# Kernel tuning notes

Measured on AMD Instinct MI355X. Metric: run time of the kernel, lower is better.

Reference implementation:

```python
import jax, jax.numpy as jnp
import numpy as np

KS = 3          # deformable kernel size
N = KS * KS     # 9 sampling points
PAD = 1         # zero padding before sampling


def setup_inputs() -> dict:
    key = jax.random.key(0)
    k = jax.random.split(key, 4)
    b, c, h, w = 8, 64, 128, 128
    x = jax.random.normal(k[0], (b, c, h, w), jnp.float32)
    # offset-prediction conv: Conv2d(c, 2*N, 3, padding=1, stride=1) with bias
    w_off = jax.random.normal(k[1], (2 * N, c, 3, 3), jnp.float32) * 0.01
    b_off = jax.random.normal(k[2], (2 * N,), jnp.float32) * 0.01
    # main conv: Conv2d(c, c, 3, stride=3, bias=None) applied to rearranged samples
    w_conv = jax.random.normal(k[3], (c, c, KS, KS), jnp.float32) * (1.0 / np.sqrt(c * N))
    return {"x": x, "w_off": w_off, "b_off": b_off, "w_conv": w_conv}


def _deform_conv2d(x, w_off, b_off, w_conv):
    b, c, h, w = x.shape
    # 1) predict offsets: (b, 2N, h, w)
    offset = jax.lax.conv_general_dilated(
        x, w_off, (1, 1), ((PAD, PAD), (PAD, PAD)),
        dimension_numbers=("NCHW", "OIHW", "NCHW"))
    offset = offset + b_off[None, :, None, None]
    offset = offset.transpose(0, 2, 3, 1)  # (b, h, w, 2N), first N = rows, last N = cols

    # 2) sampling positions p = p_0 + p_n + offset (in zero-padded coords)
    dx, dy = jnp.meshgrid(
        jnp.arange(-(KS - 1) // 2, (KS - 1) // 2 + 1),
        jnp.arange(-(KS - 1) // 2, (KS - 1) // 2 + 1), indexing="ij")
    pn_x = dx.reshape(-1).astype(x.dtype)  # (N,)
    pn_y = dy.reshape(-1).astype(x.dtype)
    r0 = jnp.arange(1, h + 1, dtype=x.dtype)  # p_0 starts at 1 (padding shift)
    c0 = jnp.arange(1, w + 1, dtype=x.dtype)
    p_x = offset[..., :N] + pn_x + r0[None, :, None, None]   # (b,h,w,N)
    p_y = offset[..., N:] + pn_y + c0[None, None, :, None]

    xp = jnp.pad(x, ((0, 0), (0, 0), (PAD, PAD), (PAD, PAD)))
    Hp, Wp = h + 2 * PAD, w + 2 * PAD

    fx = jnp.floor(p_x)
    fy = jnp.floor(p_y)
    q_lt_x = jnp.clip(fx, 0, Hp - 1).astype(jnp.int32)
    q_lt_y = jnp.clip(fy, 0, Wp - 1).astype(jnp.int32)
    q_rb_x = jnp.clip(fx + 1, 0, Hp - 1).astype(jnp.int32)
    q_rb_y = jnp.clip(fy + 1, 0, Wp - 1).astype(jnp.int32)
    p_x = jnp.clip(p_x, 0, Hp - 1)
    p_y = jnp.clip(p_y, 0, Wp - 1)

    # bilinear weights (b,h,w,N); q values are non-differentiable (int)
    g_lt = (1 + (q_lt_x - p_x)) * (1 + (q_lt_y - p_y))
    g_rb = (1 - (q_rb_x - p_x)) * (1 - (q_rb_y - p_y))
    g_lb = (1 + (q_lt_x - p_x)) * (1 - (q_rb_y - p_y))
    g_rt = (1 - (q_rb_x - p_x)) * (1 + (q_lt_y - p_y))

    xp_flat = xp.reshape(b, c, Hp * Wp)

    def gather(qx, qy):
        idx = (qx * Wp + qy).reshape(b, 1, h * w * N)
        out = jnp.take_along_axis(
            xp_flat, jnp.broadcast_to(idx, (b, c, h * w * N)), axis=2)
        return out.reshape(b, c, h, w, N)

    x_off = (g_lt[:, None] * gather(q_lt_x, q_lt_y)
             + g_rb[:, None] * gather(q_rb_x, q_rb_y)
             + g_lb[:, None] * gather(q_lt_x, q_rb_y)
             + g_rt[:, None] * gather(q_rb_x, q_lt_y))  # (b,c,h,w,N)

    # 3) final KSxKS conv with stride KS over the rearranged samples is exactly
    #    a contraction over the N sampling points (sample n = kernel tap (i,j), n=i*KS+j)
    out = jnp.einsum("bchwn,ocn->bohw", x_off, w_conv.reshape(c, c, N))
    return out


def reference(x, w_off, b_off, w_conv):
    return _deform_conv2d(x, w_off, b_off, w_conv) + x
```

## Files before the change

### kernel.cpp

```cpp
#include <hip/hip_runtime.h>


typedef _Float16 h2    __attribute__((ext_vector_type(2)));
typedef _Float16 f16x8 __attribute__((ext_vector_type(8)));
typedef float    f32x4 __attribute__((ext_vector_type(4)));

#define MFMAH(a, b, c) __builtin_amdgcn_mfma_f32_16x16x32_f16(a, b, c, 0, 0, 0)

__device__ __forceinline__ unsigned short f2h(float f) {
    return __builtin_bit_cast(unsigned short, (_Float16)f);
}
__device__ __forceinline__ float h2f_bits(unsigned u) {
    return (float)__builtin_bit_cast(_Float16, (unsigned short)(u & 0xffffu));
}
__device__ __forceinline__ unsigned dup16(float g) {
    _Float16 t = (_Float16)g;
    h2 r = {t, t};
    return __builtin_bit_cast(unsigned, r);
}

__device__ __forceinline__ void blend8(const uint4* clo, const uint4* chi, uint4 gq,
                                       f16x8& bfr0, f16x8& bfr1) {
    h2 g0 = __builtin_bit_cast(h2, gq.x), g1 = __builtin_bit_cast(h2, gq.y);
    h2 g2 = __builtin_bit_cast(h2, gq.z), g3 = __builtin_bit_cast(h2, gq.w);
    const unsigned* c0 = (const unsigned*)&clo[0];
    const unsigned* c1 = (const unsigned*)&clo[1];
    const unsigned* c2 = (const unsigned*)&clo[2];
    const unsigned* c3 = (const unsigned*)&clo[3];
    const unsigned* e0 = (const unsigned*)&chi[0];
    const unsigned* e1 = (const unsigned*)&chi[1];
    const unsigned* e2 = (const unsigned*)&chi[2];
    const unsigned* e3 = (const unsigned*)&chi[3];
    unsigned owl[4], owh[4];
#pragma unroll
    for (int d = 0; d < 4; ++d) {
        h2 sl = __builtin_bit_cast(h2, c0[d]) * g0;
        sl = __builtin_elementwise_fma(__builtin_bit_cast(h2, c1[d]), g1, sl);
        sl = __builtin_elementwise_fma(__builtin_bit_cast(h2, c2[d]), g2, sl);
        sl = __builtin_elementwise_fma(__builtin_bit_cast(h2, c3[d]), g3, sl);
        owl[d] = __builtin_bit_cast(unsigned, sl);
        h2 sh = __builtin_bit_cast(h2, e0[d]) * g0;
        sh = __builtin_elementwise_fma(__builtin_bit_cast(h2, e1[d]), g1, sh);
        sh = __builtin_elementwise_fma(__builtin_bit_cast(h2, e2[d]), g2, sh);
        sh = __builtin_elementwise_fma(__builtin_bit_cast(h2, e3[d]), g3, sh);
        owh[d] = __builtin_bit_cast(unsigned, sh);
    }
    bfr0 = __builtin_bit_cast(f16x8, *(const uint4*)owl);
    bfr1 = __builtin_bit_cast(f16x8, *(const uint4*)owh);
}

__global__ __launch_bounds__(256) void k_prep_xt(const float* __restrict__ x,
                                                 unsigned short* __restrict__ xt) {
    __shared__ float xs[64][129];
    const int bh = blockIdx.x;
    const int h = bh & 127, b = bh >> 7;
    const float* xr = x + ((size_t)b * 64 * 128 + h) * 128;
    for (int idx = threadIdx.x; idx < 8192; idx += 256) {
        int c = idx >> 7, w = idx & 127;
        xs[c][w] = xr[(size_t)c * 16384 + w];
    }
    __syncthreads();
    unsigned short* xto = xt + ((size_t)bh << 13);
    for (int j = threadIdx.x; j < 1024; j += 256) {
        int w = j >> 3, c0 = (j & 7) << 3;
        unsigned short tmp[8];
#pragma unroll
        for (int e = 0; e < 8; ++e) tmp[e] = f2h(xs[c0 + e][w]);
        *(uint4*)(xto + w * 64 + c0) = *(const uint4*)tmp;
    }
}

__global__ void k_prep_w(const float* __restrict__ w_conv, const float* __restrict__ w_off,
                         unsigned short* __restrict__ w_m2, unsigned short* __restrict__ woff2) {
    int t = blockIdx.x * 256 + threadIdx.x;
    if (t < 36864) {
        int r = t & 511;
        int fid = t >> 9;
        int l15 = r >> 5, q4 = (r >> 3) & 3, e = t & 7;
        int chunk = fid & 1, of = (fid >> 1) & 3, n = fid >> 3;
        int o = of * 16 + l15, c = chunk * 32 + q4 * 8 + e;
        w_m2[t] = f2h(w_conv[(o * 64 + c) * 9 + n]);
    }
    int t2 = t - 36864;
    if (t2 >= 0 && t2 < 18432) {
        int r = t2 & 511;
        int fid = t2 >> 9;
        int l15 = r >> 5, q4 = (r >> 3) & 3, e = t2 & 7;
        int kc = fid & 1, half = (fid >> 1) & 1, rj = fid >> 2;
        int k = half * 16 + l15, c = kc * 32 + q4 * 8 + e;
        woff2[t2] = (k < 18) ? f2h(w_off[(k * 64 + c) * 9 + rj]) : (unsigned short)0;
    }
}

__global__ __launch_bounds__(256, 2) void k_fused(
    const float* __restrict__ x, const unsigned short* __restrict__ xt,
    const unsigned short* __restrict__ w_m2, const unsigned short* __restrict__ woff2,
    const float* __restrict__ b_off, float* __restrict__ out) {

    __shared__ __align__(16) unsigned char raw[6 * 70 * 128];
    __shared__ __align__(16) _Float16 offv[64 * 24];
    __shared__ int sfb;

    const int wk = ((blockIdx.x & 7) << 8) + (blockIdx.x >> 3);
    const int b = wk >> 8, h = (wk >> 1) & 127, wt = (wk & 1) << 6;

    const int tid  = threadIdx.x;
    const int lane = tid & 63, wid = tid >> 6;
    const int l15  = lane & 15, q4 = lane >> 4;
    const int lofs = ((l15 << 2) + q4) << 3;
    const int px   = wid * 16 + l15;

    const unsigned short* xtb = xt + ((size_t)b << 20);
    const _Float16* wmh  = (const _Float16*)w_m2;
    const _Float16* wofh = (const _Float16*)woff2;

    if (tid == 0) sfb = 0;

    for (int idx = tid; idx < 3360; idx += 256) {
        int rec = idx >> 3, cc = idx & 7;
        int rl = rec / 70, col = rec - rl * 70;
        int xr = h - 2 + rl, xc = wt - 3 + col;
        uint4 v = make_uint4(0, 0, 0, 0);
        if (xr >= 0 && xr < 128 && xc >= 0 && xc < 128)
            v = *(const uint4*)(xtb + ((((size_t)xr << 7) + xc) << 6) + (cc << 3));
        *(uint4*)(raw + (rec << 7) + ((cc ^ (col & 7)) << 4)) = v;
    }
    __syncthreads();

    {
        f32x4 o0a = {0,0,0,0}, o0b = {0,0,0,0}, o1a = {0,0,0,0}, o1b = {0,0,0,0};
        f16x8 bfgA, af0A, af1A, bfgB, af0B, af1B;

#define ALOAD(s, S)                                                                      \
        {                                                                                \
            constexpr int rj = (s) >> 1, kc = (s) & 1;                                   \
            const int colw = px + (rj % 3) + 2;                                          \
            const int recb = ((rj / 3) + 1) * 70 + colw;                                 \
            bfg##S = *(const f16x8*)(raw + (recb << 7) + ((((kc << 2) + q4) ^ (colw & 7)) << 4)); \
            af0##S = *(const f16x8*)(wofh + ((((rj * 2 + 0) << 1) + kc) << 9) + lofs);   \
            af1##S = *(const f16x8*)(wofh + ((((rj * 2 + 1) << 1) + kc) << 9) + lofs);   \
        }
#define AEXEC(S, P)                                                                      \
        {                                                                                \
            o0##P = MFMAH(af0##S, bfg##S, o0##P);                                        \
            o1##P = MFMAH(af1##S, bfg##S, o1##P);                                        \
        }
        ALOAD(0, A)
        ALOAD(1, B)  AEXEC(A, a)
        ALOAD(2, A)  AEXEC(B, b)
        ALOAD(3, B)  AEXEC(A, a)
        ALOAD(4, A)  AEXEC(B, b)
        ALOAD(5, B)  AEXEC(A, a)
        ALOAD(6, A)  AEXEC(B, b)
        ALOAD(7, B)  AEXEC(A, a)
        ALOAD(8, A)  AEXEC(B, b)
        ALOAD(9, B)  AEXEC(A, a)
        ALOAD(10, A) AEXEC(B, b)
        ALOAD(11, B) AEXEC(A, a)
        ALOAD(12, A) AEXEC(B, b)
        ALOAD(13, B) AEXEC(A, a)
        ALOAD(14, A) AEXEC(B, b)
        ALOAD(15, B) AEXEC(A, a)
        ALOAD(16, A) AEXEC(B, b)
        ALOAD(17, B) AEXEC(A, a)
                     AEXEC(B, b)
#undef ALOAD
#undef AEXEC
        f32x4 o0, o1;
#pragma unroll
        for (int rg = 0; rg < 4; ++rg) { o0[rg] = o0a[rg] + o0b[rg]; o1[rg] = o1a[rg] + o1b[rg]; }
        float4 bo = *(const float4*)(b_off + (q4 << 2));
        float2 bo2 = *(const float2*)(b_off + 16);
        const float bov[4] = {bo.x, bo.y, bo.z, bo.w};
#pragma unroll
        for (int rg = 0; rg < 4; ++rg) {
            int o = (q4 << 2) + rg;
            offv[px * 24 + o] = (_Float16)(o0[rg] + bov[rg]);
            if (q4 == 0 && rg < 2) offv[px * 24 + 16 + rg] = (_Float16)(o1[rg] + (rg ? bo2.y : bo2.x));
        }
    }
    __syncthreads();

    for (int idx = tid; idx < 576; idx += 256) {
        const int n = idx >> 6, p = idx & 63;
        const int g = n / 3, dj = n % 3;
        float ox = (float)offv[p * 24 + n], oy = (float)offv[p * 24 + 9 + n];
        float pxf = (float)(h + g) + ox, pyf = (float)(wt + p + dj) + oy;
        float fx = floorf(pxf), fy = floorf(pyf);
        int wr0 = (int)fminf(fmaxf(fx, 0.f), 129.f) + 1 - h;
        int wr1 = (int)fminf(fmaxf(fx + 1.f, 0.f), 129.f) + 1 - h;
        int c0 = (int)fminf(fmaxf(fy, 0.f), 129.f) - wt + 2;
        int c1 = (int)fminf(fmaxf(fy + 1.f, 0.f), 129.f) - wt + 2;
        bool oow = ((unsigned)wr0 > 5u) | ((unsigned)wr1 > 5u) |
                   ((unsigned)c0 > 69u) | ((unsigned)c1 > 69u);
        if (oow) sfb = 1;
    }
    __syncthreads();
    const bool slow = (sfb != 0);

    const size_t obase = ((size_t)b * 64 * 128 + h) * 128 + wt + px;
    float xres[4][4];
#pragma unroll
    for (int of = 0; of < 4; ++of)
#pragma unroll
        for (int rg = 0; rg < 4; ++rg)
            xres[of][rg] = x[obase + (size_t)((of << 4) + (q4 << 2) + rg) * 16384];

    f32x4 acc[4];
#pragma unroll
    for (int of = 0; of < 4; ++of) acc[of] = (f32x4){0.f, 0.f, 0.f, 0.f};

    if (!slow) {
        const unsigned* op = (const unsigned*)(offv + px * 24);
        uint4 oA = *(const uint4*)op;
        uint4 oB = *(const uint4*)(op + 4);
        unsigned oC = op[8];
        const unsigned owr[9] = {oA.x, oA.y, oA.z, oA.w, oB.x, oB.y, oB.z, oB.w, oC};
#define OXQ(n) h2f_bits(owr[(n) >> 1] >> (((n) & 1) << 4))
#define OYQ(n) h2f_bits(owr[(9 + (n)) >> 1] >> (((9 + (n)) & 1) << 4))

        uint4 cloA[4], chiA[4], cloB[4], chiB[4];
        uint4 gqA, gqB;
        f16x8 waA[8], waB[8];

#define TAPLOAD(n, S)                                                                    \
        {                                                                                \
            constexpr int g = (n) / 3, dj = (n) % 3;                                     \
            float ox = OXQ(n), oy = OYQ(n);                                              \
            float pxf = (float)(h + g) + ox, pyf = (float)(wt + px + dj) + oy;           \
            float fx = floorf(pxf), fy = floorf(pyf);                                    \
            float qx0f = fminf(fmaxf(fx, 0.f), 129.f);                                   \
            float qx1f = fminf(fmaxf(fx + 1.f, 0.f), 129.f);                             \
            float qy0f = fminf(fmaxf(fy, 0.f), 129.f);                                   \
            float qy1f = fminf(fmaxf(fy + 1.f, 0.f), 129.f);                             \
            float pxc = fminf(fmaxf(pxf, 0.f), 129.f);                                   \
            float pyc = fminf(fmaxf(pyf, 0.f), 129.f);                                   \
            float ax0 = 1.f + (qx0f - pxc), ax1 = 1.f - (qx1f - pxc);                    \
            float ay0 = 1.f + (qy0f - pyc), ay1 = 1.f - (qy1f - pyc);                    \
            int r0 = ((int)qx0f + 1 - h) * 70, r1 = ((int)qx1f + 1 - h) * 70;            \
            int c0 = (int)qy0f - wt + 2, c1 = (int)qy1f - wt + 2;                        \
            int blt = (r0 + c0) << 7, brb = (r1 + c1) << 7;                              \
            int blb = (r0 + c1) << 7, brt = (r1 + c0) << 7;                              \
            int z0 = ((q4 ^ c0) & 7) << 4, z1 = ((q4 ^ c1) & 7) << 4;                    \
            clo##S[0] = *(const uint4*)(raw + blt + z0);                                 \
            chi##S[0] = *(const uint4*)(raw + blt + (z0 ^ 64));                          \
            clo##S[1] = *(const uint4*)(raw + brb + z1);                                 \
            chi##S[1] = *(const uint4*)(raw + brb + (z1 ^ 64));                          \
            clo##S[2] = *(const uint4*)(raw + blb + z1);                                 \
            chi##S[2] = *(const uint4*)(raw + blb + (z1 ^ 64));                          \
            chi##S[3] = *(const uint4*)(raw + brt + (z0 ^ 64));                          \
            clo##S[3] = *(const uint4*)(raw + brt + z0);                                 \
            gq##S = make_uint4(dup16(ax0 * ay0), dup16(ax1 * ay1),                       \
                               dup16(ax0 * ay1), dup16(ax1 * ay0));                      \
            const _Float16* wn = wmh + ((n) << 12);                                      \
            _Pragma("unroll")                                                            \
            for (int of = 0; of < 4; ++of) {                                             \
                wa##S[2 * of]     = *(const f16x8*)(wn + (((of << 1) + 0) << 9) + lofs); \
                wa##S[2 * of + 1] = *(const f16x8*)(wn + (((of << 1) + 1) << 9) + lofs); \
            }                                                                            \
        }

#define TAPEXEC(S)                                                                       \
        {                                                                                \
            f16x8 bfr0, bfr1;                                                            \
            blend8(clo##S, chi##S, gq##S, bfr0, bfr1);                                   \
            _Pragma("unroll")                                                            \
            for (int of = 0; of < 4; ++of) {                                             \
                acc[of] = MFMAH(wa##S[2 * of],     bfr0, acc[of]);                       \
                acc[of] = MFMAH(wa##S[2 * of + 1], bfr1, acc[of]);                       \
            }                                                                            \
        }

        TAPLOAD(0, A)
        TAPLOAD(1, B) TAPEXEC(A)
        TAPLOAD(2, A) TAPEXEC(B)
        TAPLOAD(3, B) TAPEXEC(A)
        TAPLOAD(4, A) TAPEXEC(B)
        TAPLOAD(5, B) TAPEXEC(A)
        TAPLOAD(6, A) TAPEXEC(B)
        TAPLOAD(7, B) TAPEXEC(A)
        TAPLOAD(8, A) TAPEXEC(B)
                      TAPEXEC(A)
#undef TAPLOAD
#undef TAPEXEC
#undef OXQ
#undef OYQ
    } else {
        for (int n = 0; n < 9; ++n) {
            const int g = n / 3, dj = n % 3;
            float ox = (float)offv[px * 24 + n], oy = (float)offv[px * 24 + 9 + n];
            float pxf = (float)(h + g) + ox, pyf = (float)(wt + px + dj) + oy;
            float fx = floorf(pxf), fy = floorf(pyf);
            float qx0f = fminf(fmaxf(fx, 0.f), 129.f);
            float qx1f = fminf(fmaxf(fx + 1.f, 0.f), 129.f);
            float qy0f = fminf(fmaxf(fy, 0.f), 129.f);
            float qy1f = fminf(fmaxf(fy + 1.f, 0.f), 129.f);
            float pxc = fminf(fmaxf(pxf, 0.f), 129.f);
            float pyc = fminf(fmaxf(pyf, 0.f), 129.f);
            float ax0 = 1.f + (qx0f - pxc), ax1 = 1.f - (qx1f - pxc);
            float ay0 = 1.f + (qy0f - pyc), ay1 = 1.f - (qy1f - pyc);
            int qx[2] = {(int)qx0f, (int)qx1f};
            int qy[2] = {(int)qy0f, (int)qy1f};
            uint4 clo[4], chi[4];
            const int rsel[4] = {0, 1, 0, 1}, csel[4] = {0, 1, 1, 0};
#pragma unroll
            for (int j = 0; j < 4; ++j) {
                int rx = qx[rsel[j]], ry = qy[csel[j]];
                bool v = (rx >= 1) & (rx <= 128) & (ry >= 1) & (ry <= 128);
                clo[j] = make_uint4(0, 0, 0, 0);
                chi[j] = make_uint4(0, 0, 0, 0);
                if (v) {
                    const unsigned short* gp = xtb + ((((size_t)(rx - 1) << 7) + (ry - 1)) << 6);
                    clo[j] = *(const uint4*)(gp + (q4 << 3));
                    chi[j] = *(const uint4*)(gp + (q4 << 3) + 32);
                }
            }
            uint4 gq = make_uint4(dup16(ax0 * ay0), dup16(ax1 * ay1),
                                  dup16(ax0 * ay1), dup16(ax1 * ay0));
            f16x8 bfr0, bfr1;
            blend8(clo, chi, gq, bfr0, bfr1);
            const _Float16* wn = wmh + (n << 12);
#pragma unroll
            for (int of = 0; of < 4; ++of) {
                f16x8 a0 = *(const f16x8*)(wn + (((of << 1) + 0) << 9) + lofs);
                f16x8 a1 = *(const f16x8*)(wn + (((of << 1) + 1) << 9) + lofs);
                acc[of] = MFMAH(a0, bfr0, acc[of]);
                acc[of] = MFMAH(a1, bfr1, acc[of]);
            }
        }
    }

#pragma unroll
    for (int of = 0; of < 4; ++of)
#pragma unroll
        for (int rg = 0; rg < 4; ++rg)
            out[obase + (size_t)((of << 4) + (q4 << 2) + rg) * 16384] = acc[of][rg] + xres[of][rg];
}

extern "C" void kernel_launch(void* const* d_in, const int* in_sizes, int n_in,
                              void* d_out, int out_size, void* d_ws, size_t ws_size,
                              hipStream_t stream) {
    const float* x      = (const float*)d_in[0];
    const float* w_off  = (const float*)d_in[1];
    const float* b_off  = (const float*)d_in[2];
    const float* w_conv = (const float*)d_in[3];

    unsigned short* xt    = (unsigned short*)d_ws;
    unsigned short* w_m2  = xt + (size_t)8 * 128 * 128 * 64;
    unsigned short* woff2 = w_m2 + 9 * 64 * 64;

    hipLaunchKernelGGL(k_prep_xt, dim3(1024), dim3(256), 0, stream, x, xt);
    hipLaunchKernelGGL(k_prep_w,  dim3(216),  dim3(256), 0, stream, w_conv, w_off, w_m2, woff2);
    hipLaunchKernelGGL(k_fused,   dim3(2048), dim3(256), 0, stream,
                       x, xt, w_m2, woff2, b_off, (float*)d_out);
}
```

Measured before the change: 91.60 us.

## Widen fused block to a full image row with rolling LDS row buffer and LDS weights

Each block now covers a full 128-pixel output row with 512 threads instead of a 64-wide half row. It keeps a 4-slot circular buffer of input rows in LDS, refilled with prefetched rows between tap groups, and stages both weight sets in LDS instead of reading them from global memory. The fast-path check now only tests row bounds, since the full row width is resident. This removes duplicated halo loads and global weight reads, but uses about 145 KB of dynamic LDS and adds extra block-wide barriers, which limits occupancy to one block per CU.

Result: faster. 79.38 us (-13.3%).

```diff
diff --git a/kernel.cpp b/kernel.cpp
--- a/kernel.cpp
+++ b/kernel.cpp
@@ -6,6 +6,13 @@
 typedef float    f32x4 __attribute__((ext_vector_type(4)));
 
 #define MFMAH(a, b, c) __builtin_amdgcn_mfma_f32_16x16x32_f16(a, b, c, 0, 0, 0)
+
+#define RAW_SZ  68608
+#define W_OFF   68608
+#define W_SZ    73728
+#define OFV_OFF 142336
+#define SFB_OFF 148480
+#define LDS_TOT 148496
 
 __device__ __forceinline__ unsigned short f2h(float f) {
     return __builtin_bit_cast(unsigned short, (_Float16)f);
@@ -92,17 +99,19 @@
     }
 }
 
-__global__ __launch_bounds__(256, 2) void k_fused(
+__global__ __launch_bounds__(512, 2) void k_fused(
     const float* __restrict__ x, const unsigned short* __restrict__ xt,
-    const unsigned short* __restrict__ w_m2, const unsigned short* __restrict__ woff2,
+    const unsigned short* __restrict__ w_m2g, const unsigned short* __restrict__ woff2g,
     const float* __restrict__ b_off, float* __restrict__ out) {
 
-    __shared__ __align__(16) unsigned char raw[6 * 70 * 128];
-    __shared__ __align__(16) _Float16 offv[64 * 24];
-    __shared__ int sfb;
-
-    const int wk = ((blockIdx.x & 7) << 8) + (blockIdx.x >> 3);
-    const int b = wk >> 8, h = (wk >> 1) & 127, wt = (wk & 1) << 6;
+    extern __shared__ __align__(16) unsigned char lds[];
+    unsigned char* raw  = lds;
+    _Float16*      wlds = (_Float16*)(lds + W_OFF);
+    _Float16*      offv = (_Float16*)(lds + OFV_OFF);
+    int*           sfbp = (int*)(lds + SFB_OFF);
+
+    const int wk = ((blockIdx.x & 7) << 7) | (blockIdx.x >> 3);
+    const int b = wk >> 7, h = wk & 127;
 
     const int tid  = threadIdx.x;
     const int lane = tid & 63, wid = tid >> 6;
@@ -111,20 +120,21 @@
     const int px   = wid * 16 + l15;
 
     const unsigned short* xtb = xt + ((size_t)b << 20);
-    const _Float16* wmh  = (const _Float16*)w_m2;
-    const _Float16* wofh = (const _Float16*)woff2;
-
-    if (tid == 0) sfb = 0;
-
-    for (int idx = tid; idx < 3360; idx += 256) {
+
+    if (tid == 0) *sfbp = 0;
+
+    for (int idx = tid; idx < 4288; idx += 512) {
         int rec = idx >> 3, cc = idx & 7;
-        int rl = rec / 70, col = rec - rl * 70;
-        int xr = h - 2 + rl, xc = wt - 3 + col;
+        int rl = rec / 134, col = rec - rl * 134;
+        int xr = h - 2 + rl, xc = col - 3;
         uint4 v = make_uint4(0, 0, 0, 0);
         if (xr >= 0 && xr < 128 && xc >= 0 && xc < 128)
             v = *(const uint4*)(xtb + ((((size_t)xr << 7) + xc) << 6) + (cc << 3));
-        *(uint4*)(raw + (rec << 7) + ((cc ^ (col & 7)) << 4)) = v;
-    }
+        int slot = (xr + 4) & 3;
+        *(uint4*)(raw + ((slot * 134 + col) << 7) + ((cc ^ (col & 7)) << 4)) = v;
+    }
+    for (int idx = tid; idx < 2304; idx += 512)
+        ((uint4*)wlds)[idx] = ((const uint4*)woff2g)[idx];
     __syncthreads();
 
     {
@@ -135,10 +145,10 @@
         {                                                                                \
             constexpr int rj = (s) >> 1, kc = (s) & 1;                                   \
             const int colw = px + (rj % 3) + 2;                                          \
-            const int recb = ((rj / 3) + 1) * 70 + colw;                                 \
-            bfg##S = *(const f16x8*)(raw + (recb << 7) + ((((kc << 2) + q4) ^ (colw & 7)) << 4)); \
-            af0##S = *(const f16x8*)(wofh + ((((rj * 2 + 0) << 1) + kc) << 9) + lofs);   \
-            af1##S = *(const f16x8*)(wofh + ((((rj * 2 + 1) << 1) + kc) << 9) + lofs);   \
+            const int slt  = (h + (rj / 3) + 3) & 3;                                     \
+            bfg##S = *(const f16x8*)(raw + ((slt * 134 + colw) << 7) + ((((kc << 2) + q4) ^ (colw & 7)) << 4)); \
+            af0##S = *(const f16x8*)(wlds + ((((rj * 2 + 0) << 1) + kc) << 9) + lofs);   \
+            af1##S = *(const f16x8*)(wlds + ((((rj * 2 + 1) << 1) + kc) << 9) + lofs);   \
         }
 #define AEXEC(S, P)                                                                      \
         {                                                                                \
@@ -166,45 +176,40 @@
                      AEXEC(B, b)
 #undef ALOAD
 #undef AEXEC
-        f32x4 o0, o1;
-#pragma unroll
-        for (int rg = 0; rg < 4; ++rg) { o0[rg] = o0a[rg] + o0b[rg]; o1[rg] = o1a[rg] + o1b[rg]; }
         float4 bo = *(const float4*)(b_off + (q4 << 2));
         float2 bo2 = *(const float2*)(b_off + 16);
         const float bov[4] = {bo.x, bo.y, bo.z, bo.w};
 #pragma unroll
         for (int rg = 0; rg < 4; ++rg) {
             int o = (q4 << 2) + rg;
-            offv[px * 24 + o] = (_Float16)(o0[rg] + bov[rg]);
-            if (q4 == 0 && rg < 2) offv[px * 24 + 16 + rg] = (_Float16)(o1[rg] + (rg ? bo2.y : bo2.x));
+            offv[px * 24 + o] = (_Float16)(o0a[rg] + o0b[rg] + bov[rg]);
+            if (q4 == 0 && rg < 2)
+                offv[px * 24 + 16 + rg] = (_Float16)(o1a[rg] + o1b[rg] + (rg ? bo2.y : bo2.x));
         }
     }
     __syncthreads();
 
-    for (int idx = tid; idx < 576; idx += 256) {
-        const int n = idx >> 6, p = idx & 63;
-        const int g = n / 3, dj = n % 3;
-        float ox = (float)offv[p * 24 + n], oy = (float)offv[p * 24 + 9 + n];
-        float pxf = (float)(h + g) + ox, pyf = (float)(wt + p + dj) + oy;
-        float fx = floorf(pxf), fy = floorf(pyf);
-        int wr0 = (int)fminf(fmaxf(fx, 0.f), 129.f) + 1 - h;
-        int wr1 = (int)fminf(fmaxf(fx + 1.f, 0.f), 129.f) + 1 - h;
-        int c0 = (int)fminf(fmaxf(fy, 0.f), 129.f) - wt + 2;
-        int c1 = (int)fminf(fmaxf(fy + 1.f, 0.f), 129.f) - wt + 2;
-        bool oow = ((unsigned)wr0 > 5u) | ((unsigned)wr1 > 5u) |
-                   ((unsigned)c0 > 69u) | ((unsigned)c1 > 69u);
-        if (oow) sfb = 1;
-    }
-    __syncthreads();
-    const bool slow = (sfb != 0);
-
-    const size_t obase = ((size_t)b * 64 * 128 + h) * 128 + wt + px;
+    for (int idx = tid; idx < 4608; idx += 512)
+        ((uint4*)wlds)[idx] = ((const uint4*)w_m2g)[idx];
+    for (int idx = tid; idx < 1152; idx += 512) {
+        int n = idx % 9, p = idx / 9;
+        int g = n / 3;
+        float ox = (float)offv[p * 24 + n];
+        float pxf = (float)(h + g) + ox;
+        float fx = floorf(pxf);
+        int t0 = (int)fminf(fmaxf(fx, 0.f), 129.f) + 1 - h - g;
+        int t1 = (int)fminf(fmaxf(fx + 1.f, 0.f), 129.f) + 1 - h - g;
+        if (((unsigned)t0 > 3u) | ((unsigned)t1 > 3u)) *sfbp = 1;
+    }
+    const size_t obase = ((size_t)b << 20) + h * 128 + px;
     float xres[4][4];
 #pragma unroll
     for (int of = 0; of < 4; ++of)
 #pragma unroll
         for (int rg = 0; rg < 4; ++rg)
             xres[of][rg] = x[obase + (size_t)((of << 4) + (q4 << 2) + rg) * 16384];
+    __syncthreads();
+    const bool slow = (*sfbp != 0);
 
     f32x4 acc[4];
 #pragma unroll
@@ -222,12 +227,39 @@
         uint4 cloA[4], chiA[4], cloB[4], chiB[4];
         uint4 gqA, gqB;
         f16x8 waA[8], waB[8];
+        uint4 pf[3];
+        int prec[3], pcc[3];
+
+#define PREF(ROW)                                                                        \
+        {                                                                                \
+            _Pragma("unroll")                                                            \
+            for (int k = 0; k < 3; ++k) {                                                \
+                int idx = tid + (k << 9);                                                \
+                bool v = idx < 1072;                                                     \
+                int rec = idx >> 3;                                                      \
+                pcc[k] = idx & 7;                                                        \
+                int xc = rec - 3;                                                        \
+                uint4 vv = make_uint4(0, 0, 0, 0);                                       \
+                if (v && (ROW) < 128 && xc >= 0 && xc < 128)                             \
+                    vv = *(const uint4*)(xtb + ((((size_t)(ROW) << 7) + xc) << 6) + (pcc[k] << 3)); \
+                prec[k] = v ? rec : -1;                                                  \
+                pf[k] = vv;                                                              \
+            }                                                                            \
+        }
+#define WRB(ROW)                                                                         \
+        {                                                                                \
+            const int slt = ((ROW) + 4) & 3;                                             \
+            _Pragma("unroll")                                                            \
+            for (int k = 0; k < 3; ++k)                                                  \
+                if (prec[k] >= 0)                                                        \
+                    *(uint4*)(raw + ((slt * 134 + prec[k]) << 7) + ((pcc[k] ^ (prec[k] & 7)) << 4)) = pf[k]; \
+        }
 
 #define TAPLOAD(n, S)                                                                    \
         {                                                                                \
             constexpr int g = (n) / 3, dj = (n) % 3;                                     \
             float ox = OXQ(n), oy = OYQ(n);                                              \
-            float pxf = (float)(h + g) + ox, pyf = (float)(wt + px + dj) + oy;           \
+            float pxf = (float)(h + g) + ox, pyf = (float)(px + dj) + oy;                \
             float fx = floorf(pxf), fy = floorf(pyf);                                    \
             float qx0f = fminf(fmaxf(fx, 0.f), 129.f);                                   \
             float qx1f = fminf(fmaxf(fx + 1.f, 0.f), 129.f);                             \
@@ -237,8 +269,8 @@
             float pyc = fminf(fmaxf(pyf, 0.f), 129.f);                                   \
             float ax0 = 1.f + (qx0f - pxc), ax1 = 1.f - (qx1f - pxc);                    \
             float ay0 = 1.f + (qy0f - pyc), ay1 = 1.f - (qy1f - pyc);                    \
-            int r0 = ((int)qx0f + 1 - h) * 70, r1 = ((int)qx1f + 1 - h) * 70;            \
-            int c0 = (int)qy0f - wt + 2, c1 = (int)qy1f - wt + 2;                        \
+            int r0 = (((int)qx0f + 3) & 3) * 134, r1 = (((int)qx1f + 3) & 3) * 134;      \
+            int c0 = (int)qy0f + 2, c1 = (int)qy1f + 2;                                  \
             int blt = (r0 + c0) << 7, brb = (r1 + c1) << 7;                              \
             int blb = (r0 + c1) << 7, brt = (r1 + c0) << 7;                              \
             int z0 = ((q4 ^ c0) & 7) << 4, z1 = ((q4 ^ c1) & 7) << 4;                    \
@@ -248,18 +280,16 @@
             chi##S[1] = *(const uint4*)(raw + brb + (z1 ^ 64));                          \
             clo##S[2] = *(const uint4*)(raw + blb + z1);                                 \
             chi##S[2] = *(const uint4*)(raw + blb + (z1 ^ 64));                          \
+            clo##S[3] = *(const uint4*)(raw + brt + z0);                                 \
             chi##S[3] = *(const uint4*)(raw + brt + (z0 ^ 64));                          \
-            clo##S[3] = *(const uint4*)(raw + brt + z0);                                 \
             gq##S = make_uint4(dup16(ax0 * ay0), dup16(ax1 * ay1),                       \
                                dup16(ax0 * ay1), dup16(ax1 * ay0));                      \
-            const _Float16* wn = wmh + ((n) << 12);                                      \
             _Pragma("unroll")                                                            \
             for (int of = 0; of < 4; ++of) {                                             \
-                wa##S[2 * of]     = *(const f16x8*)(wn + (((of << 1) + 0) << 9) + lofs); \
-                wa##S[2 * of + 1] = *(const f16x8*)(wn + (((of << 1) + 1) << 9) + lofs); \
+                wa##S[2 * of]     = *(const f16x8*)(wlds + (((n) * 8 + of * 2 + 0) << 9) + lofs); \
+                wa##S[2 * of + 1] = *(const f16x8*)(wlds + (((n) * 8 + of * 2 + 1) << 9) + lofs); \
             }                                                                            \
         }
-
 #define TAPEXEC(S)                                                                       \
         {                                                                                \
             f16x8 bfr0, bfr1;                                                            \
@@ -271,25 +301,37 @@
             }                                                                            \
         }
 
+        PREF(h + 2)
         TAPLOAD(0, A)
         TAPLOAD(1, B) TAPEXEC(A)
         TAPLOAD(2, A) TAPEXEC(B)
-        TAPLOAD(3, B) TAPEXEC(A)
-        TAPLOAD(4, A) TAPEXEC(B)
-        TAPLOAD(5, B) TAPEXEC(A)
-        TAPLOAD(6, A) TAPEXEC(B)
+                      TAPEXEC(A)
+        __syncthreads();
+        WRB(h + 2)
+        __syncthreads();
+        PREF(h + 3)
+        TAPLOAD(3, A)
+        TAPLOAD(4, B) TAPEXEC(A)
+        TAPLOAD(5, A) TAPEXEC(B)
+                      TAPEXEC(A)
+        __syncthreads();
+        WRB(h + 3)
+        __syncthreads();
+        TAPLOAD(6, A)
         TAPLOAD(7, B) TAPEXEC(A)
         TAPLOAD(8, A) TAPEXEC(B)
                       TAPEXEC(A)
 #undef TAPLOAD
 #undef TAPEXEC
+#undef PREF
+#undef WRB
 #undef OXQ
 #undef OYQ
     } else {
         for (int n = 0; n < 9; ++n) {
             const int g = n / 3, dj = n % 3;
             float ox = (float)offv[px * 24 + n], oy = (float)offv[px * 24 + 9 + n];
-            float pxf = (float)(h + g) + ox, pyf = (float)(wt + px + dj) + oy;
+            float pxf = (float)(h + g) + ox, pyf = (float)(px + dj) + oy;
             float fx = floorf(pxf), fy = floorf(pyf);
             float qx0f = fminf(fmaxf(fx, 0.f), 129.f);
             float qx1f = fminf(fmaxf(fx + 1.f, 0.f), 129.f);
@@ -319,11 +361,10 @@
                                   dup16(ax0 * ay1), dup16(ax1 * ay0));
             f16x8 bfr0, bfr1;
             blend8(clo, chi, gq, bfr0, bfr1);
-            const _Float16* wn = wmh + (n << 12);
 #pragma unroll
             for (int of = 0; of < 4; ++of) {
-                f16x8 a0 = *(const f16x8*)(wn + (((of << 1) + 0) << 9) + lofs);
-                f16x8 a1 = *(const f16x8*)(wn + (((of << 1) + 1) << 9) + lofs);
+                f16x8 a0 = *(const f16x8*)(wlds + ((n * 8 + of * 2 + 0) << 9) + lofs);
+                f16x8 a1 = *(const f16x8*)(wlds + ((n * 8 + of * 2 + 1) << 9) + lofs);
                 acc[of] = MFMAH(a0, bfr0, acc[of]);
                 acc[of] = MFMAH(a1, bfr1, acc[of]);
             }
@@ -349,8 +390,11 @@
     unsigned short* w_m2  = xt + (size_t)8 * 128 * 128 * 64;
     unsigned short* woff2 = w_m2 + 9 * 64 * 64;
 
+    hipFuncSetAttribute((const void*)k_fused,
+                        hipFuncAttributeMaxDynamicSharedMemorySize, LDS_TOT);
+
     hipLaunchKernelGGL(k_prep_xt, dim3(1024), dim3(256), 0, stream, x, xt);
     hipLaunchKernelGGL(k_prep_w,  dim3(216),  dim3(256), 0, stream, w_conv, w_off, w_m2, woff2);
-    hipLaunchKernelGGL(k_fused,   dim3(2048), dim3(256), 0, stream,
+    hipLaunchKernelGGL(k_fused,   dim3(1024), dim3(512), LDS_TOT, stream,
                        x, xt, w_m2, woff2, b_off, (float*)d_out);
 }
```
